# Optimization experiments

Measured on AMD Instinct MI355X. Metric: run time of the kernel, lower is better.

The kernel has to match this reference:

```python
import jax, jax.numpy as jnp
import numpy as np

ALPHA = 0.2  # LeakyReLU negative slope


def setup_inputs() -> dict:
    key = jax.random.key(0)
    k_h, k_adj, k_a1, k_a2 = jax.random.split(key, 4)
    B, N, D = 8, 2048, 128
    h = jax.random.normal(k_h, (B, N, D), dtype=jnp.float32)
    adj = jax.random.randint(k_adj, (B, N, N), 0, 2, dtype=jnp.int32)
    # attention parameters a1, a2: shape (D, 1) as in the original layer
    a1 = jax.random.normal(k_a1, (D, 1), dtype=jnp.float32) * (1.0 / np.sqrt(D))
    a2 = jax.random.normal(k_a2, (D, 1), dtype=jnp.float32) * (1.0 / np.sqrt(D))
    return {"h": h, "adj": adj, "a1": a1, "a2": a2}


def reference(h, adj, a1, a2):
    # h: [B, N, D]; adj: [B, N, N] (int mask); a1, a2: [D, 1]
    f1 = h @ a1                                  # [B, N, 1] per-source score
    f2 = h @ a2                                  # [B, N, 1] per-target score
    logits = f1 + jnp.swapaxes(f2, 1, 2)         # broadcast -> [B, N, N]
    logits = jnp.where(logits > 0, logits, ALPHA * logits)  # LeakyReLU
    logits = jnp.where(adj > 0, logits, -jnp.inf)            # adjacency mask
    prob = jax.nn.softmax(logits, axis=2)        # [B, N, N]
    h_prime = jnp.einsum('bij,bjd->bid', prob, h)  # weighted aggregation
    return jax.nn.elu(h_prime)                   # concat=True branch
```

## Files before the change

kernel.cpp:

```cpp
#include <hip/hip_runtime.h>
#include <hip/hip_bf16.h>
#include <math.h>

#define BB 8
#define NN 2048
#define DD 128
#define ALPHA 0.2f

typedef __attribute__((ext_vector_type(8))) short short8;
typedef __attribute__((ext_vector_type(4))) float f32x4;

__device__ inline unsigned short bf16_rne(float v) {
    unsigned int x = __float_as_uint(v);
    unsigned int r = x + 0x7FFFu + ((x >> 16) & 1u);
    return (unsigned short)(r >> 16);
}
__device__ inline float bf16_back(unsigned short u) {
    return __uint_as_float(((unsigned int)u) << 16);
}

__global__ __launch_bounds__(256) void pack_kernel(const float* __restrict__ h,
                                                   const float* __restrict__ a1,
                                                   const float* __restrict__ a2,
                                                   float* __restrict__ f1,
                                                   float* __restrict__ f2,
                                                   unsigned short* __restrict__ panel) {
    __shared__ float hs[32][DD];
    int blk = blockIdx.x;
    int b   = blk >> 6;
    int ks  = blk & 63;
    int r0  = ks * 32;
    int t   = threadIdx.x;

    const float* hb = h + ((size_t)b * NN + r0) * DD;
#pragma unroll
    for (int m = 0; m < 4; ++m) {
        int off = t * 4 + m * 1024;
        *reinterpret_cast<float4*>(&hs[0][0] + off) =
            *reinterpret_cast<const float4*>(hb + off);
    }
    __syncthreads();

    {
        int row = t >> 3, d0 = (t & 7) * 16;
        float s1 = 0.f, s2 = 0.f;
#pragma unroll
        for (int q = 0; q < 4; ++q) {
            float4 hv  = *reinterpret_cast<const float4*>(&hs[row][d0 + q * 4]);
            float4 av1 = *reinterpret_cast<const float4*>(a1 + d0 + q * 4);
            float4 av2 = *reinterpret_cast<const float4*>(a2 + d0 + q * 4);
            s1 += hv.x * av1.x + hv.y * av1.y + hv.z * av1.z + hv.w * av1.w;
            s2 += hv.x * av2.x + hv.y * av2.y + hv.z * av2.z + hv.w * av2.w;
        }
#pragma unroll
        for (int off = 1; off < 8; off <<= 1) {
            s1 += __shfl_xor(s1, off, 64);
            s2 += __shfl_xor(s2, off, 64);
        }
        if ((t & 7) == 0) {
            f1[b * NN + r0 + row] = s1;
            f2[b * NN + r0 + row] = s2;
        }
    }

    {
        int n = t >> 1;
        size_t base = (((size_t)b * 64 + ks) * 128 + n) * 32;
#pragma unroll
        for (int cc = 0; cc < 2; ++cc) {
            int c = (t & 1) * 2 + cc;
            unsigned short u[8];
#pragma unroll
            for (int e = 0; e < 8; ++e) u[e] = bf16_rne(hs[c * 8 + e][n]);
            short8 v;
#pragma unroll
            for (int e = 0; e < 8; ++e) v[e] = (short)u[e];
            *reinterpret_cast<short8*>(panel + base + (size_t)c * 8) = v;
        }
    }
}

__global__ __launch_bounds__(256, 2) void gat_mfma(const int* __restrict__ adj,
                                                   const float* __restrict__ f1,
                                                   const float* __restrict__ f2,
                                                   const unsigned short* __restrict__ panel,
                                                   float* __restrict__ out) {
    __shared__ float buf[2][32][132];
    __shared__ float sden[4][32];

    int blk  = blockIdx.x;
    int b    = blk & 7;
    int tile = blk >> 3;
    int i0   = tile * 32;
    int t    = threadIdx.x;
    int w    = t >> 6, l = t & 63;
    int lr   = l & 15, lc = l >> 4;

    const int* adjb = adj + (size_t)b * NN * NN;
    const unsigned short* pb = panel + (size_t)b * (64 * 128 * 32);
    const float* f2b = f2 + b * NN;
    float f1r0 = f1[b * NN + i0 + lr];
    float f1r1 = f1[b * NN + i0 + 16 + lr];

    f32x4 acc[2][8];
#pragma unroll
    for (int mt = 0; mt < 2; ++mt)
#pragma unroll
        for (int nt = 0; nt < 8; ++nt) acc[mt][nt] = (f32x4){0.f, 0.f, 0.f, 0.f};
    float sacc0 = 0.f, sacc1 = 0.f;

    int kbase = w * 512;
    for (int ks = 0; ks < 16; ++ks) {
        int k0 = kbase + ks * 32;
        int jb = k0 + lc * 8;
        float4 f2a = *reinterpret_cast<const float4*>(f2b + jb);
        float4 f2c = *reinterpret_cast<const float4*>(f2b + jb + 4);
        const int* ar0 = adjb + (size_t)(i0 + lr) * NN + jb;
        const int* ar1 = ar0 + (size_t)16 * NN;
        int4 a00 = *reinterpret_cast<const int4*>(ar0);
        int4 a01 = *reinterpret_cast<const int4*>(ar0 + 4);
        int4 a10 = *reinterpret_cast<const int4*>(ar1);
        int4 a11 = *reinterpret_cast<const int4*>(ar1 + 4);
        const unsigned short* pk = pb + (size_t)(k0 >> 5) * 4096 + lr * 32 + lc * 8;
        short8 bf[8];
#pragma unroll
        for (int nt = 0; nt < 8; ++nt)
            bf[nt] = *reinterpret_cast<const short8*>(pk + nt * 512);

        float f2v[8] = {f2a.x, f2a.y, f2a.z, f2a.w, f2c.x, f2c.y, f2c.z, f2c.w};
        int aj0[8] = {a00.x, a00.y, a00.z, a00.w, a01.x, a01.y, a01.z, a01.w};
        int aj1[8] = {a10.x, a10.y, a10.z, a10.w, a11.x, a11.y, a11.z, a11.w};

        short8 af0, af1;
#pragma unroll
        for (int e = 0; e < 8; ++e) {
            float x0 = f1r0 + f2v[e];
            float e0 = fmaxf(x0, ALPHA * x0);
            float w0 = (aj0[e] > 0) ? __expf(e0) : 0.f;
            unsigned short u0 = bf16_rne(w0);
            sacc0 += bf16_back(u0);
            af0[e] = (short)u0;

            float x1 = f1r1 + f2v[e];
            float e1 = fmaxf(x1, ALPHA * x1);
            float w1 = (aj1[e] > 0) ? __expf(e1) : 0.f;
            unsigned short u1 = bf16_rne(w1);
            sacc1 += bf16_back(u1);
            af1[e] = (short)u1;
        }
#pragma unroll
        for (int nt = 0; nt < 8; ++nt) {
            acc[0][nt] = __builtin_amdgcn_mfma_f32_16x16x32_bf16(af0, bf[nt], acc[0][nt], 0, 0, 0);
            acc[1][nt] = __builtin_amdgcn_mfma_f32_16x16x32_bf16(af1, bf[nt], acc[1][nt], 0, 0, 0);
        }
    }

    sacc0 += __shfl_xor(sacc0, 16, 64); sacc0 += __shfl_xor(sacc0, 32, 64);
    sacc1 += __shfl_xor(sacc1, 16, 64); sacc1 += __shfl_xor(sacc1, 32, 64);
    if (l < 16) { sden[w][l] = sacc0; sden[w][16 + l] = sacc1; }

    float* mybuf = &buf[w >> 1][0][0];
    if ((w & 1) == 0) {
#pragma unroll
        for (int mt = 0; mt < 2; ++mt)
#pragma unroll
            for (int nt = 0; nt < 8; ++nt) {
                float* p = mybuf + (mt * 16 + lc * 4) * 132 + nt * 16 + lr;
#pragma unroll
                for (int r = 0; r < 4; ++r) p[r * 132] = acc[mt][nt][r];
            }
    }
    __syncthreads();
    if (w & 1) {
#pragma unroll
        for (int mt = 0; mt < 2; ++mt)
#pragma unroll
            for (int nt = 0; nt < 8; ++nt) {
                float* p = mybuf + (mt * 16 + lc * 4) * 132 + nt * 16 + lr;
#pragma unroll
                for (int r = 0; r < 4; ++r) p[r * 132] += acc[mt][nt][r];
            }
    }
    __syncthreads();

    {
        int row = t >> 3, col0 = (t & 7) * 16;
        float den = sden[0][row] + sden[1][row] + sden[2][row] + sden[3][row];
        float inv = 1.0f / den;
        float* ob = out + ((size_t)b * NN + i0 + row) * DD;
#pragma unroll
        for (int q = 0; q < 4; ++q) {
            int col = col0 + q * 4;
            const float* p0 = &buf[0][row][col];
            const float* p1 = &buf[1][row][col];
            float4 v0 = *reinterpret_cast<const float4*>(p0);
            float4 v1 = *reinterpret_cast<const float4*>(p1);
            float r0 = (v0.x + v1.x) * inv;
            float r1 = (v0.y + v1.y) * inv;
            float r2 = (v0.z + v1.z) * inv;
            float r3 = (v0.w + v1.w) * inv;
            r0 = (r0 > 0.f) ? r0 : expm1f(r0);
            r1 = (r1 > 0.f) ? r1 : expm1f(r1);
            r2 = (r2 > 0.f) ? r2 : expm1f(r2);
            r3 = (r3 > 0.f) ? r3 : expm1f(r3);
            *reinterpret_cast<float4*>(ob + col) = make_float4(r0, r1, r2, r3);
        }
    }
}

extern "C" void kernel_launch(void* const* d_in, const int* in_sizes, int n_in,
                              void* d_out, int out_size, void* d_ws, size_t ws_size,
                              hipStream_t stream) {
    const float* h   = (const float*)d_in[0];
    const int*   adj = (const int*)d_in[1];
    const float* a1  = (const float*)d_in[2];
    const float* a2  = (const float*)d_in[3];
    float* out = (float*)d_out;

    float* f1 = (float*)d_ws;
    float* f2 = f1 + BB * NN;
    unsigned short* panel = (unsigned short*)(f2 + BB * NN);

    pack_kernel<<<BB * 64, 256, 0, stream>>>(h, a1, a2, f1, f2, panel);
    gat_mfma<<<BB * 64, 256, 0, stream>>>(adj, f1, f2, panel, out);
}
```

Before: 219.4 us.

## Halve row tile to 16, prefetch adjacency, use exp2 with prescaled scores

The main kernel now processes 16 rows per block instead of 32. This doubles the grid to 1024 blocks, halves the accumulator registers, and raises the launch bound to 4 blocks per CU for more occupancy and latency hiding. Adjacency and f2 loads for the next k-step are software-prefetched into registers, and the loop is fully unrolled. Scores are prescaled by log2(e) in the pack kernel so the exponent uses the hardware exp2 instruction. In exchange, each panel (h) load now feeds half as many MFMAs, which doubles panel traffic per output row.

Measured after the change: 243.5 us. +11.0%, slower.

```diff
diff --git a/kernel.cpp b/kernel.cpp
--- a/kernel.cpp
+++ b/kernel.cpp
@@ -6,6 +6,7 @@
 #define NN 2048
 #define DD 128
 #define ALPHA 0.2f
+#define LOG2E 1.4426950408889634f
 
 typedef __attribute__((ext_vector_type(8))) short short8;
 typedef __attribute__((ext_vector_type(4))) float f32x4;
@@ -58,8 +59,8 @@
             s2 += __shfl_xor(s2, off, 64);
         }
         if ((t & 7) == 0) {
-            f1[b * NN + r0 + row] = s1;
-            f2[b * NN + r0 + row] = s2;
+            f1[b * NN + r0 + row] = s1 * LOG2E;
+            f2[b * NN + r0 + row] = s2 * LOG2E;
         }
     }
 
@@ -69,132 +70,120 @@
 #pragma unroll
         for (int cc = 0; cc < 2; ++cc) {
             int c = (t & 1) * 2 + cc;
-            unsigned short u[8];
-#pragma unroll
-            for (int e = 0; e < 8; ++e) u[e] = bf16_rne(hs[c * 8 + e][n]);
             short8 v;
 #pragma unroll
-            for (int e = 0; e < 8; ++e) v[e] = (short)u[e];
+            for (int e = 0; e < 8; ++e) v[e] = (short)bf16_rne(hs[c * 8 + e][n]);
             *reinterpret_cast<short8*>(panel + base + (size_t)c * 8) = v;
         }
     }
 }
 
-__global__ __launch_bounds__(256, 2) void gat_mfma(const int* __restrict__ adj,
+__global__ __launch_bounds__(256, 4) void gat_mfma(const int* __restrict__ adj,
                                                    const float* __restrict__ f1,
                                                    const float* __restrict__ f2,
                                                    const unsigned short* __restrict__ panel,
                                                    float* __restrict__ out) {
-    __shared__ float buf[2][32][132];
-    __shared__ float sden[4][32];
+    __shared__ float buf[2][16][132];
+    __shared__ float sden[4][16];
 
     int blk  = blockIdx.x;
     int b    = blk & 7;
     int tile = blk >> 3;
-    int i0   = tile * 32;
+    int i0   = tile * 16;
     int t    = threadIdx.x;
     int w    = t >> 6, l = t & 63;
     int lr   = l & 15, lc = l >> 4;
 
-    const int* adjb = adj + (size_t)b * NN * NN;
     const unsigned short* pb = panel + (size_t)b * (64 * 128 * 32);
     const float* f2b = f2 + b * NN;
-    float f1r0 = f1[b * NN + i0 + lr];
-    float f1r1 = f1[b * NN + i0 + 16 + lr];
-
-    f32x4 acc[2][8];
-#pragma unroll
-    for (int mt = 0; mt < 2; ++mt)
-#pragma unroll
-        for (int nt = 0; nt < 8; ++nt) acc[mt][nt] = (f32x4){0.f, 0.f, 0.f, 0.f};
-    float sacc0 = 0.f, sacc1 = 0.f;
+    const int* arow  = adj + (size_t)b * NN * NN + (size_t)(i0 + lr) * NN;
+    float f1r = f1[b * NN + i0 + lr];
+
+    f32x4 acc[8];
+#pragma unroll
+    for (int nt = 0; nt < 8; ++nt) acc[nt] = (f32x4){0.f, 0.f, 0.f, 0.f};
+    float sacc = 0.f;
 
     int kbase = w * 512;
+
+    int jb0 = kbase + lc * 8;
+    int4   ajN0 = *reinterpret_cast<const int4*>(arow + jb0);
+    int4   ajN1 = *reinterpret_cast<const int4*>(arow + jb0 + 4);
+    float4 f2N0 = *reinterpret_cast<const float4*>(f2b + jb0);
+    float4 f2N1 = *reinterpret_cast<const float4*>(f2b + jb0 + 4);
+
+#pragma unroll
     for (int ks = 0; ks < 16; ++ks) {
         int k0 = kbase + ks * 32;
-        int jb = k0 + lc * 8;
-        float4 f2a = *reinterpret_cast<const float4*>(f2b + jb);
-        float4 f2c = *reinterpret_cast<const float4*>(f2b + jb + 4);
-        const int* ar0 = adjb + (size_t)(i0 + lr) * NN + jb;
-        const int* ar1 = ar0 + (size_t)16 * NN;
-        int4 a00 = *reinterpret_cast<const int4*>(ar0);
-        int4 a01 = *reinterpret_cast<const int4*>(ar0 + 4);
-        int4 a10 = *reinterpret_cast<const int4*>(ar1);
-        int4 a11 = *reinterpret_cast<const int4*>(ar1 + 4);
+        int4 a0 = ajN0, a1 = ajN1;
+        float4 g0 = f2N0, g1 = f2N1;
+
         const unsigned short* pk = pb + (size_t)(k0 >> 5) * 4096 + lr * 32 + lc * 8;
         short8 bf[8];
 #pragma unroll
         for (int nt = 0; nt < 8; ++nt)
             bf[nt] = *reinterpret_cast<const short8*>(pk + nt * 512);
 
-        float f2v[8] = {f2a.x, f2a.y, f2a.z, f2a.w, f2c.x, f2c.y, f2c.z, f2c.w};
-        int aj0[8] = {a00.x, a00.y, a00.z, a00.w, a01.x, a01.y, a01.z, a01.w};
-        int aj1[8] = {a10.x, a10.y, a10.z, a10.w, a11.x, a11.y, a11.z, a11.w};
-
-        short8 af0, af1;
+        if (ks < 15) {
+            int jn = k0 + 32 + lc * 8;
+            ajN0 = *reinterpret_cast<const int4*>(arow + jn);
+            ajN1 = *reinterpret_cast<const int4*>(arow + jn + 4);
+            f2N0 = *reinterpret_cast<const float4*>(f2b + jn);
+            f2N1 = *reinterpret_cast<const float4*>(f2b + jn + 4);
+        }
+
+        float f2v[8] = {g0.x, g0.y, g0.z, g0.w, g1.x, g1.y, g1.z, g1.w};
+        int   aj[8]  = {a0.x, a0.y, a0.z, a0.w, a1.x, a1.y, a1.z, a1.w};
+
+        short8 af;
 #pragma unroll
         for (int e = 0; e < 8; ++e) {
-            float x0 = f1r0 + f2v[e];
-            float e0 = fmaxf(x0, ALPHA * x0);
-            float w0 = (aj0[e] > 0) ? __expf(e0) : 0.f;
-            unsigned short u0 = bf16_rne(w0);
-            sacc0 += bf16_back(u0);
-            af0[e] = (short)u0;
-
-            float x1 = f1r1 + f2v[e];
-            float e1 = fmaxf(x1, ALPHA * x1);
-            float w1 = (aj1[e] > 0) ? __expf(e1) : 0.f;
-            unsigned short u1 = bf16_rne(w1);
-            sacc1 += bf16_back(u1);
-            af1[e] = (short)u1;
-        }
-#pragma unroll
-        for (int nt = 0; nt < 8; ++nt) {
-            acc[0][nt] = __builtin_amdgcn_mfma_f32_16x16x32_bf16(af0, bf[nt], acc[0][nt], 0, 0, 0);
-            acc[1][nt] = __builtin_amdgcn_mfma_f32_16x16x32_bf16(af1, bf[nt], acc[1][nt], 0, 0, 0);
-        }
-    }
-
-    sacc0 += __shfl_xor(sacc0, 16, 64); sacc0 += __shfl_xor(sacc0, 32, 64);
-    sacc1 += __shfl_xor(sacc1, 16, 64); sacc1 += __shfl_xor(sacc1, 32, 64);
-    if (l < 16) { sden[w][l] = sacc0; sden[w][16 + l] = sacc1; }
+            float x  = f1r + f2v[e];
+            float ee = fmaxf(x, ALPHA * x);
+            float wv = (aj[e] > 0) ? __builtin_amdgcn_exp2f(ee) : 0.f;
+            unsigned short u = bf16_rne(wv);
+            sacc += bf16_back(u);
+            af[e] = (short)u;
+        }
+#pragma unroll
+        for (int nt = 0; nt < 8; ++nt)
+            acc[nt] = __builtin_amdgcn_mfma_f32_16x16x32_bf16(af, bf[nt], acc[nt], 0, 0, 0);
+    }
+
+    sacc += __shfl_xor(sacc, 16, 64);
+    sacc += __shfl_xor(sacc, 32, 64);
+    if (l < 16) sden[w][l] = sacc;
 
     float* mybuf = &buf[w >> 1][0][0];
     if ((w & 1) == 0) {
 #pragma unroll
-        for (int mt = 0; mt < 2; ++mt)
-#pragma unroll
-            for (int nt = 0; nt < 8; ++nt) {
-                float* p = mybuf + (mt * 16 + lc * 4) * 132 + nt * 16 + lr;
-#pragma unroll
-                for (int r = 0; r < 4; ++r) p[r * 132] = acc[mt][nt][r];
-            }
+        for (int nt = 0; nt < 8; ++nt) {
+            float* p = mybuf + (lc * 4) * 132 + nt * 16 + lr;
+#pragma unroll
+            for (int r = 0; r < 4; ++r) p[r * 132] = acc[nt][r];
+        }
     }
     __syncthreads();
     if (w & 1) {
 #pragma unroll
-        for (int mt = 0; mt < 2; ++mt)
-#pragma unroll
-            for (int nt = 0; nt < 8; ++nt) {
-                float* p = mybuf + (mt * 16 + lc * 4) * 132 + nt * 16 + lr;
-#pragma unroll
-                for (int r = 0; r < 4; ++r) p[r * 132] += acc[mt][nt][r];
-            }
+        for (int nt = 0; nt < 8; ++nt) {
+            float* p = mybuf + (lc * 4) * 132 + nt * 16 + lr;
+#pragma unroll
+            for (int r = 0; r < 4; ++r) p[r * 132] += acc[nt][r];
+        }
     }
     __syncthreads();
 
     {
-        int row = t >> 3, col0 = (t & 7) * 16;
+        int row = t >> 4, col0 = (t & 15) * 8;
         float den = sden[0][row] + sden[1][row] + sden[2][row] + sden[3][row];
         float inv = 1.0f / den;
         float* ob = out + ((size_t)b * NN + i0 + row) * DD;
 #pragma unroll
-        for (int q = 0; q < 4; ++q) {
+        for (int q = 0; q < 2; ++q) {
             int col = col0 + q * 4;
-            const float* p0 = &buf[0][row][col];
-            const float* p1 = &buf[1][row][col];
-            float4 v0 = *reinterpret_cast<const float4*>(p0);
-            float4 v1 = *reinterpret_cast<const float4*>(p1);
+            float4 v0 = *reinterpret_cast<const float4*>(&buf[0][row][col]);
+            float4 v1 = *reinterpret_cast<const float4*>(&buf[1][row][col]);
             float r0 = (v0.x + v1.x) * inv;
             float r1 = (v0.y + v1.y) * inv;
             float r2 = (v0.z + v1.z) * inv;
@@ -222,5 +211,5 @@
     unsigned short* panel = (unsigned short*)(f2 + BB * NN);
 
     pack_kernel<<<BB * 64, 256, 0, stream>>>(h, a1, a2, f1, f2, panel);
-    gat_mfma<<<BB * 64, 256, 0, stream>>>(adj, f1, f2, panel, out);
-}
+    gat_mfma<<<BB * 128, 256, 0, stream>>>(adj, f1, f2, panel, out);
+}
```
